# Kernel tuning notes

Measured on AMD Instinct MI355X. Metric: run time of the kernel, lower is better.

The kernel has to match this reference:

```python
import jax, jax.numpy as jnp
import numpy as np

N_NODES = 100000
N_EDGES = 3200000
IN_CH = 256
HID = 256   # 2 * out_channels
OUT = 128


def _gcn_norm(edge_index, n):
    # PyG GCNConv normalization: add self-loops, norm = d^-1/2[src] * d^-1/2[dst]
    src, dst = edge_index[0], edge_index[1]
    loops = jnp.arange(n, dtype=src.dtype)
    src = jnp.concatenate([src, loops])
    dst = jnp.concatenate([dst, loops])
    ones = jnp.ones_like(dst, dtype=jnp.float32)
    deg = jax.ops.segment_sum(ones, dst, num_segments=n)
    dinv = jnp.where(deg > 0, jax.lax.rsqrt(deg), 0.0)
    norm = dinv[src] * dinv[dst]
    return src, dst, norm


def _gcn_conv(x, W, b, src, dst, norm, n):
    h = x @ W                              # [N, F_out] dense transform first (F_out <= F_in)
    msg = h[src] * norm[:, None]           # gather + scale  [E+N, F_out]
    out = jax.ops.segment_sum(msg, dst, num_segments=n)  # scatter-add
    return out + b


def setup_inputs() -> dict:
    key = jax.random.key(0)
    k1, k2, k3, k4 = jax.random.split(key, 4)
    x = jax.random.normal(k1, (N_NODES, IN_CH), dtype=jnp.float32)
    edge_index = jax.random.randint(k2, (2, N_EDGES), 0, N_NODES, dtype=jnp.int64)
    # Glorot-style init for weights, zero bias (PyG GCNConv defaults)
    W1 = jax.random.normal(k3, (IN_CH, HID), dtype=jnp.float32) * (1.0 / np.sqrt(IN_CH))
    b1 = jnp.zeros((HID,), dtype=jnp.float32)
    W2 = jax.random.normal(k4, (HID, OUT), dtype=jnp.float32) * (1.0 / np.sqrt(HID))
    b2 = jnp.zeros((OUT,), dtype=jnp.float32)
    return {"x": x, "edge_index": edge_index, "W1": W1, "b1": b1, "W2": W2, "b2": b2}


def reference(x, edge_index, W1, b1, W2, b2):
    n = x.shape[0]
    src, dst, norm = _gcn_norm(edge_index, n)  # cached=True: shared across both layers
    h = _gcn_conv(x, W1, b1, src, dst, norm, n)
    h = jax.nn.relu(h)
    z = _gcn_conv(h, W2, b2, src, dst, norm, n)
    return z
```

## Files before the change

kernel.cpp:

```cpp
#include <hip/hip_runtime.h>
#include <cstdio>


#define NPB 256
#define PCHUNK 8192

typedef _Float16 half4v __attribute__((ext_vector_type(4)));
typedef _Float16 half8v __attribute__((ext_vector_type(8)));
typedef float    f32x4  __attribute__((ext_vector_type(4)));
typedef float    f32x8  __attribute__((ext_vector_type(8)));

__global__ __launch_bounds__(256) void k_bhist(const int* __restrict__ dst,
                                               int* __restrict__ bcnt,
                                               int e, int nb) {
  __shared__ int h[512];
  for (int i = threadIdx.x; i < nb; i += 256) h[i] = 0;
  __syncthreads();
  int c0 = blockIdx.x * PCHUNK;
  int c1 = min(c0 + PCHUNK, e);
  for (int i = c0 + threadIdx.x; i < c1; i += 256)
    atomicAdd(&h[dst[i] >> 8], 1);
  __syncthreads();
  for (int i = threadIdx.x; i < nb; i += 256)
    if (h[i]) atomicAdd(&bcnt[i], h[i]);
}

__global__ __launch_bounds__(512) void k_bscan(const int* __restrict__ bcnt,
                                               int* __restrict__ bbase,
                                               int* __restrict__ gcur, int nb) {
  __shared__ int sm[512];
  int tid = threadIdx.x;
  sm[tid] = (tid < nb) ? bcnt[tid] : 0;
  __syncthreads();
  for (int d = 1; d < 512; d <<= 1) {
    int t = (tid >= d) ? sm[tid - d] : 0;
    __syncthreads();
    sm[tid] += t;
    __syncthreads();
  }
  int ex = (tid == 0) ? 0 : sm[tid - 1];
  if (tid < nb) {
    bbase[tid] = ex;
    gcur[tid] = ex;
  }
  if (tid == nb) bbase[nb] = sm[nb - 1];
}

__global__ __launch_bounds__(256) void k_partition(const int* __restrict__ src,
                                                   const int* __restrict__ dst,
                                                   int* __restrict__ gcur,
                                                   uint2* __restrict__ tmp,
                                                   int e, int nb) {
  __shared__ int hist[512];
  __shared__ int base[512];
  for (int i = threadIdx.x; i < nb; i += 256) hist[i] = 0;
  __syncthreads();
  int c0 = blockIdx.x * PCHUNK;
  int c1 = min(c0 + PCHUNK, e);
  for (int i = c0 + threadIdx.x; i < c1; i += 256)
    atomicAdd(&hist[dst[i] >> 8], 1);
  __syncthreads();
  for (int i = threadIdx.x; i < nb; i += 256) {
    int c = hist[i];
    base[i] = c ? atomicAdd(&gcur[i], c) : 0;
    hist[i] = 0;
  }
  __syncthreads();
  for (int i = c0 + threadIdx.x; i < c1; i += 256) {
    int d = dst[i];
    int b = d >> 8;
    int pos = base[b] + atomicAdd(&hist[b], 1);
    uint2 v;
    v.x = (unsigned)src[i];
    v.y = (unsigned)d;
    tmp[pos] = v;
  }
}

__global__ __launch_bounds__(256) void k_bucket(const uint2* __restrict__ tmp,
                                                const int* __restrict__ bbase,
                                                int* __restrict__ off,
                                                float* __restrict__ dinv,
                                                int* __restrict__ esrc, int n) {
  __shared__ int lcnt[NPB];
  __shared__ int lsum[NPB];
  __shared__ int lcur[NPB];
  const int b = blockIdx.x;
  const int tid = threadIdx.x;
  const int r0 = b << 8;
  const int nn = min(NPB, n - r0);
  const int lo = bbase[b], hi = bbase[b + 1];

  lcnt[tid] = 0;
  __syncthreads();
  for (int i = lo + tid; i < hi; i += 256)
    atomicAdd(&lcnt[tmp[i].y & (NPB - 1)], 1);
  __syncthreads();
  lsum[tid] = lcnt[tid];
  __syncthreads();
  for (int d = 1; d < NPB; d <<= 1) {
    int t = (tid >= d) ? lsum[tid - d] : 0;
    __syncthreads();
    lsum[tid] += t;
    __syncthreads();
  }
  int ex = (tid == 0) ? 0 : lsum[tid - 1];
  if (tid < nn) {
    off[r0 + tid] = lo + ex;
    dinv[r0 + tid] = rsqrtf((float)(lcnt[tid] + 1));
    lcur[tid] = lo + ex;
  }
  if (r0 + nn == n && tid == 0) off[n] = hi;
  __syncthreads();
  for (int i = lo + tid; i < hi; i += 256) {
    uint2 t2 = tmp[i];
    int pos = atomicAdd(&lcur[t2.y & (NPB - 1)], 1);
    esrc[pos] = (int)t2.x;
  }
}

__global__ __launch_bounds__(256) void k_castWT(const float* __restrict__ W,
                                                _Float16* __restrict__ WhT,
                                                _Float16* __restrict__ WlT,
                                                int K, int N) {
  int i = blockIdx.x * 256 + threadIdx.x;
  if (i >= K * N) return;
  int n = i % N, k = i / N;
  float v = W[i];
  _Float16 h = (_Float16)v;
  WhT[(size_t)n * K + k] = h;
  WlT[(size_t)n * K + k] = (_Float16)(v - (float)h);
}

__global__ __launch_bounds__(256, 2) void k_gemm1(
    const float* __restrict__ A, const _Float16* __restrict__ BhT,
    const _Float16* __restrict__ BlT, _Float16* __restrict__ C,
    int M, int N, int K) {
  __shared__ _Float16 Ah[128][40];
  __shared__ _Float16 Al[128][40];

  const int tid = threadIdx.x;
  const int bm = blockIdx.x * 128;

  const int arow = tid >> 1;
  const int acol = (tid & 1) * 16;
  const bool avalid = (bm + arow) < M;
  const float* aptr = A + (size_t)(bm + arow) * K + acol;

  const int wave = tid >> 6, lane = tid & 63;
  const int wm = (wave & 1) * 64, wn = (wave >> 1) * 128;
  const int lr = lane & 15, quad = lane >> 4;

  const _Float16* bh0 = BhT + (size_t)(wn + lr) * K + quad * 8;
  const _Float16* bl0 = BlT + (size_t)(wn + lr) * K + quad * 8;

  f32x4 acc[4][8] = {};

  for (int k0 = 0; k0 < K; k0 += 32) {
    __syncthreads();
    if (avalid) {
#pragma unroll
      for (int ii = 0; ii < 4; ++ii) {
        f32x4 v = *(const f32x4*)(aptr + k0 + ii * 4);
        half4v hv, lv;
#pragma unroll
        for (int j = 0; j < 4; ++j) {
          hv[j] = (_Float16)v[j];
          lv[j] = (_Float16)(v[j] - (float)hv[j]);
        }
        *(half4v*)&Ah[arow][acol + ii * 4] = hv;
        *(half4v*)&Al[arow][acol + ii * 4] = lv;
      }
    } else {
      half4v z = {};
#pragma unroll
      for (int ii = 0; ii < 4; ++ii) {
        *(half4v*)&Ah[arow][acol + ii * 4] = z;
        *(half4v*)&Al[arow][acol + ii * 4] = z;
      }
    }
    __syncthreads();

    half8v af[4], alf[4];
#pragma unroll
    for (int mi = 0; mi < 4; ++mi) {
      af[mi] = *(const half8v*)&Ah[wm + mi * 16 + lr][quad * 8];
      alf[mi] = *(const half8v*)&Al[wm + mi * 16 + lr][quad * 8];
    }
#pragma unroll
    for (int ni = 0; ni < 8; ++ni) {
      half8v bh = *(const half8v*)(bh0 + (size_t)(ni * 16) * K + k0);
      half8v bl = *(const half8v*)(bl0 + (size_t)(ni * 16) * K + k0);
#pragma unroll
      for (int mi = 0; mi < 4; ++mi) {
        acc[mi][ni] = __builtin_amdgcn_mfma_f32_16x16x32_f16(
            af[mi], bh, acc[mi][ni], 0, 0, 0);
        acc[mi][ni] = __builtin_amdgcn_mfma_f32_16x16x32_f16(
            af[mi], bl, acc[mi][ni], 0, 0, 0);
        acc[mi][ni] = __builtin_amdgcn_mfma_f32_16x16x32_f16(
            alf[mi], bh, acc[mi][ni], 0, 0, 0);
      }
    }
  }

#pragma unroll
  for (int mi = 0; mi < 4; ++mi)
#pragma unroll
    for (int r = 0; r < 4; ++r) {
      int row = bm + wm + mi * 16 + quad * 4 + r;
      if (row < M) {
#pragma unroll
        for (int ni = 0; ni < 8; ++ni)
          C[(size_t)row * N + wn + ni * 16 + lr] = (_Float16)acc[mi][ni][r];
      }
    }
}

template <typename AT, int NTERMS>
__global__ __launch_bounds__(256, 2) void k_gemm_mfma(
    const AT* __restrict__ A, const _Float16* __restrict__ BhT,
    const _Float16* __restrict__ BlT, _Float16* __restrict__ C,
    int M, int N, int K) {
  constexpr bool SPLITA = (NTERMS == 3);
  __shared__ _Float16 Ah[128][40];
  __shared__ _Float16 Al[SPLITA ? 128 : 1][40];

  const int tid = threadIdx.x;
  const int bm = blockIdx.x * 128;
  const int bn = blockIdx.y * 128;

  const int arow = tid >> 1;
  const int acol = (tid & 1) * 16;
  const bool avalid = (bm + arow) < M;
  const AT* aptr = A + (size_t)(bm + arow) * K + acol;

  const int wave = tid >> 6, lane = tid & 63;
  const int wm = (wave & 1) * 64, wn = (wave >> 1) * 64;
  const int lr = lane & 15, quad = lane >> 4;

  const _Float16* bh0 = BhT + (size_t)(bn + wn + lr) * K + quad * 8;
  const _Float16* bl0 = BlT + (size_t)(bn + wn + lr) * K + quad * 8;

  f32x4 acc[4][4] = {};

  for (int k0 = 0; k0 < K; k0 += 32) {
    __syncthreads();
    if (avalid) {
#pragma unroll
      for (int ii = 0; ii < 4; ++ii) {
        if constexpr (SPLITA) {
          f32x4 v = *(const f32x4*)(aptr + k0 + ii * 4);
          half4v hv, lv;
#pragma unroll
          for (int j = 0; j < 4; ++j) {
            hv[j] = (_Float16)v[j];
            lv[j] = (_Float16)(v[j] - (float)hv[j]);
          }
          *(half4v*)&Ah[arow][acol + ii * 4] = hv;
          *(half4v*)&Al[arow][acol + ii * 4] = lv;
        } else {
          half4v v = *(const half4v*)(aptr + k0 + ii * 4);
          *(half4v*)&Ah[arow][acol + ii * 4] = v;
        }
      }
    } else {
      half4v z = {};
#pragma unroll
      for (int ii = 0; ii < 4; ++ii) {
        *(half4v*)&Ah[arow][acol + ii * 4] = z;
        if constexpr (SPLITA) *(half4v*)&Al[arow][acol + ii * 4] = z;
      }
    }
    __syncthreads();

    half8v af[4], alf[4], bhf[4], blf[4];
#pragma unroll
    for (int mi = 0; mi < 4; ++mi) {
      af[mi] = *(const half8v*)&Ah[wm + mi * 16 + lr][quad * 8];
      if constexpr (SPLITA)
        alf[mi] = *(const half8v*)&Al[wm + mi * 16 + lr][quad * 8];
    }
#pragma unroll
    for (int ni = 0; ni < 4; ++ni) {
      bhf[ni] = *(const half8v*)(bh0 + (size_t)(ni * 16) * K + k0);
      blf[ni] = *(const half8v*)(bl0 + (size_t)(ni * 16) * K + k0);
    }
#pragma unroll
    for (int mi = 0; mi < 4; ++mi)
#pragma unroll
      for (int ni = 0; ni < 4; ++ni) {
        acc[mi][ni] = __builtin_amdgcn_mfma_f32_16x16x32_f16(
            af[mi], bhf[ni], acc[mi][ni], 0, 0, 0);
        acc[mi][ni] = __builtin_amdgcn_mfma_f32_16x16x32_f16(
            af[mi], blf[ni], acc[mi][ni], 0, 0, 0);
        if constexpr (SPLITA)
          acc[mi][ni] = __builtin_amdgcn_mfma_f32_16x16x32_f16(
              alf[mi], bhf[ni], acc[mi][ni], 0, 0, 0);
      }
  }

#pragma unroll
  for (int mi = 0; mi < 4; ++mi)
#pragma unroll
    for (int r = 0; r < 4; ++r) {
      int row = bm + wm + mi * 16 + quad * 4 + r;
      if (row < M) {
#pragma unroll
        for (int ni = 0; ni < 4; ++ni)
          C[(size_t)row * N + bn + wn + ni * 16 + lr] =
              (_Float16)acc[mi][ni][r];
      }
    }
}

template <int C, bool RELU, typename OutT>
__global__ __launch_bounds__(256) void k_agg(const _Float16* __restrict__ h,
                                             const int* __restrict__ esrc,
                                             const int* __restrict__ off,
                                             const float* __restrict__ dinv,
                                             const float* __restrict__ bias,
                                             OutT* __restrict__ out, int n) {
  constexpr int LPE = C / 8;
  constexpr int EPL = 64 / LPE;
  constexpr int U = 4;
  int gwave = (blockIdx.x * 256 + threadIdx.x) >> 6;
  int lane = threadIdx.x & 63;
  if (gwave >= n) return;
  const int i = gwave;
  const int eslot = lane / LPE;
  const int sub = lane % LPE;
  const float di = dinv[i];
  const _Float16* hb = h + sub * 8;

  f32x8 acc = {};
  if (eslot == 0)
    acc = di * __builtin_convertvector(*(const half8v*)(hb + (size_t)i * C),
                                       f32x8);

  int e = off[i];
  const int e1 = off[i + 1];
  for (; e + U * EPL <= e1; e += U * EPL) {
    int s[U];
#pragma unroll
    for (int g = 0; g < U; ++g) s[g] = esrc[e + g * EPL + eslot];
    float w[U];
    half8v v[U];
#pragma unroll
    for (int g = 0; g < U; ++g) {
      w[g] = dinv[s[g]];
      v[g] = *(const half8v*)(hb + (size_t)s[g] * C);
    }
#pragma unroll
    for (int g = 0; g < U; ++g)
      acc += w[g] * __builtin_convertvector(v[g], f32x8);
  }
  for (; e < e1; e += EPL) {
    int eg = e + eslot;
    if (eg < e1) {
      int s = esrc[eg];
      acc += dinv[s] * __builtin_convertvector(
                           *(const half8v*)(hb + (size_t)s * C), f32x8);
    }
  }

#pragma unroll
  for (int j = 0; j < 8; ++j) {
    float t = acc[j];
#pragma unroll
    for (int m = LPE; m < 64; m <<= 1) t += __shfl_xor(t, m);
    acc[j] = t;
  }

  if (eslot == 0) {
    f32x8 bv = *(const f32x8*)(bias + sub * 8);
    f32x8 r = acc * di + bv;
    if (RELU) {
#pragma unroll
      for (int j = 0; j < 8; ++j) r[j] = fmaxf(r[j], 0.f);
    }
    if constexpr (sizeof(OutT) == 2) {
      *(half8v*)(out + (size_t)i * C + sub * 8) =
          __builtin_convertvector(r, half8v);
    } else {
      *(f32x8*)(out + (size_t)i * C + sub * 8) = r;
    }
  }
}

extern "C" void kernel_launch(void* const* d_in, const int* in_sizes, int n_in,
                              void* d_out, int out_size, void* d_ws, size_t ws_size,
                              hipStream_t stream) {
  const float* x  = (const float*)d_in[0];
  const int*   ei = (const int*)d_in[1];
  const float* W1 = (const float*)d_in[2];
  const float* b1 = (const float*)d_in[3];
  const float* W2 = (const float*)d_in[4];
  const float* b2 = (const float*)d_in[5];
  float* out = (float*)d_out;

  const int IN_CH = 256, HID = 256, OUT = 128;
  const int N = in_sizes[0] / IN_CH;
  const int E = in_sizes[1] / 2;
  const int* src = ei;
  const int* dst = ei + E;
  const int NB = (N + NPB - 1) / NPB;

  char* p = (char*)d_ws;
  auto alloc = [&](size_t bytes) {
    void* r = (void*)p;
    p += (bytes + 255) & ~(size_t)255;
    return r;
  };
  _Float16* h1   = (_Float16*)alloc((size_t)N * HID * 2);
  _Float16* h1r  = (_Float16*)alloc((size_t)N * HID * 2);
  int*      esrc = (int*)alloc((size_t)E * 4);
  uint2*    tmp  = (uint2*)alloc((size_t)E * 8);
  int*      off  = (int*)alloc((size_t)(N + 1) * 4);
  float*    dinv = (float*)alloc((size_t)N * 4);
  int*      bcnt = (int*)alloc((size_t)(NB + 1) * 4);
  int*      bbase= (int*)alloc((size_t)(NB + 1) * 4);
  int*      gcur = (int*)alloc((size_t)(NB + 1) * 4);
  _Float16* w1h  = (_Float16*)alloc((size_t)IN_CH * HID * 2);
  _Float16* w1l  = (_Float16*)alloc((size_t)IN_CH * HID * 2);
  _Float16* w2h  = (_Float16*)alloc((size_t)HID * OUT * 2);
  _Float16* w2l  = (_Float16*)alloc((size_t)HID * OUT * 2);
  if ((size_t)(p - (char*)d_ws) > ws_size) {
    fprintf(stderr, "kernel_launch: ws too small (need %zu, have %zu)\n",
            (size_t)(p - (char*)d_ws), ws_size);
    return;
  }

  const int nBlkP = (E + PCHUNK - 1) / PCHUNK;

  hipMemsetAsync(bcnt, 0, (size_t)(NB + 1) * 4, stream);
  k_bhist<<<nBlkP, 256, 0, stream>>>(dst, bcnt, E, NB);
  k_bscan<<<1, 512, 0, stream>>>(bcnt, bbase, gcur, NB);
  k_partition<<<nBlkP, 256, 0, stream>>>(src, dst, gcur, tmp, E, NB);
  k_bucket<<<NB, 256, 0, stream>>>(tmp, bbase, off, dinv, esrc, N);
  k_castWT<<<(IN_CH * HID + 255) / 256, 256, 0, stream>>>(W1, w1h, w1l, IN_CH, HID);
  k_castWT<<<(HID * OUT + 255) / 256, 256, 0, stream>>>(W2, w2h, w2l, HID, OUT);
  k_gemm1<<<(N + 127) / 128, 256, 0, stream>>>(x, w1h, w1l, h1, N, HID, IN_CH);
  int aggBlk = (N + 3) / 4;
  k_agg<256, true, _Float16><<<aggBlk, 256, 0, stream>>>(h1, esrc, off, dinv, b1, h1r, N);
  dim3 g2((N + 127) / 128, OUT / 128);
  k_gemm_mfma<_Float16, 2><<<g2, 256, 0, stream>>>(h1r, w2h, w2l, h1, N, OUT, HID);
  k_agg<128, false, float><<<aggBlk, 256, 0, stream>>>(h1, esrc, off, dinv, b2, out, N);
}
```

Baseline: 744.3 us.

## Split GCN aggregation into 64-channel passes and use finer dst buckets

The neighbour aggregation now runs as several launches, each gathering only a 64-channel slice of the features. This shrinks the per-pass gather working set so more of the random row gathers can hit in cache. The price is rereading the edge lists and dinv once per pass and paying extra launch overhead. The CSR build also moves to 64-node buckets with smaller partition chunks, and the bucket scan now handles more buckets than threads.

```diff
diff --git a/kernel.cpp b/kernel.cpp
--- a/kernel.cpp
+++ b/kernel.cpp
@@ -2,8 +2,9 @@
 #include <cstdio>
 
 
-#define NPB 256
-#define PCHUNK 8192
+#define NPB 64
+#define PCHUNK 2048
+#define MAXB 1664
 
 typedef _Float16 half4v __attribute__((ext_vector_type(4)));
 typedef _Float16 half8v __attribute__((ext_vector_type(8)));
@@ -13,13 +14,13 @@
 __global__ __launch_bounds__(256) void k_bhist(const int* __restrict__ dst,
                                                int* __restrict__ bcnt,
                                                int e, int nb) {
-  __shared__ int h[512];
+  __shared__ int h[MAXB];
   for (int i = threadIdx.x; i < nb; i += 256) h[i] = 0;
   __syncthreads();
   int c0 = blockIdx.x * PCHUNK;
   int c1 = min(c0 + PCHUNK, e);
   for (int i = c0 + threadIdx.x; i < c1; i += 256)
-    atomicAdd(&h[dst[i] >> 8], 1);
+    atomicAdd(&h[dst[i] >> 6], 1);
   __syncthreads();
   for (int i = threadIdx.x; i < nb; i += 256)
     if (h[i]) atomicAdd(&bcnt[i], h[i]);
@@ -27,10 +28,16 @@
 
 __global__ __launch_bounds__(512) void k_bscan(const int* __restrict__ bcnt,
                                                int* __restrict__ bbase,
-                                               int* __restrict__ gcur, int nb) {
+                                               int* __restrict__ gcur,
+                                               int nb) {
   __shared__ int sm[512];
-  int tid = threadIdx.x;
-  sm[tid] = (tid < nb) ? bcnt[tid] : 0;
+  const int tid = threadIdx.x;
+  const int chunk = (nb + 511) >> 9;
+  const int c0 = min(tid * chunk, nb);
+  const int c1 = min(c0 + chunk, nb);
+  int sum = 0;
+  for (int j = c0; j < c1; ++j) sum += bcnt[j];
+  sm[tid] = sum;
   __syncthreads();
   for (int d = 1; d < 512; d <<= 1) {
     int t = (tid >= d) ? sm[tid - d] : 0;
@@ -38,12 +45,13 @@
     sm[tid] += t;
     __syncthreads();
   }
-  int ex = (tid == 0) ? 0 : sm[tid - 1];
-  if (tid < nb) {
-    bbase[tid] = ex;
-    gcur[tid] = ex;
-  }
-  if (tid == nb) bbase[nb] = sm[nb - 1];
+  int run = (tid == 0) ? 0 : sm[tid - 1];
+  for (int j = c0; j < c1; ++j) {
+    bbase[j] = run;
+    gcur[j] = run;
+    run += bcnt[j];
+  }
+  if (tid == 511) bbase[nb] = run;
 }
 
 __global__ __launch_bounds__(256) void k_partition(const int* __restrict__ src,
@@ -51,14 +59,14 @@
                                                    int* __restrict__ gcur,
                                                    uint2* __restrict__ tmp,
                                                    int e, int nb) {
-  __shared__ int hist[512];
-  __shared__ int base[512];
+  __shared__ int hist[MAXB];
+  __shared__ int base[MAXB];
   for (int i = threadIdx.x; i < nb; i += 256) hist[i] = 0;
   __syncthreads();
   int c0 = blockIdx.x * PCHUNK;
   int c1 = min(c0 + PCHUNK, e);
   for (int i = c0 + threadIdx.x; i < c1; i += 256)
-    atomicAdd(&hist[dst[i] >> 8], 1);
+    atomicAdd(&hist[dst[i] >> 6], 1);
   __syncthreads();
   for (int i = threadIdx.x; i < nb; i += 256) {
     int c = hist[i];
@@ -68,7 +76,7 @@
   __syncthreads();
   for (int i = c0 + threadIdx.x; i < c1; i += 256) {
     int d = dst[i];
-    int b = d >> 8;
+    int b = d >> 6;
     int pos = base[b] + atomicAdd(&hist[b], 1);
     uint2 v;
     v.x = (unsigned)src[i];
@@ -87,24 +95,24 @@
   __shared__ int lcur[NPB];
   const int b = blockIdx.x;
   const int tid = threadIdx.x;
-  const int r0 = b << 8;
+  const int r0 = b << 6;
   const int nn = min(NPB, n - r0);
   const int lo = bbase[b], hi = bbase[b + 1];
 
-  lcnt[tid] = 0;
+  if (tid < NPB) lcnt[tid] = 0;
   __syncthreads();
   for (int i = lo + tid; i < hi; i += 256)
     atomicAdd(&lcnt[tmp[i].y & (NPB - 1)], 1);
   __syncthreads();
-  lsum[tid] = lcnt[tid];
+  if (tid < NPB) lsum[tid] = lcnt[tid];
   __syncthreads();
   for (int d = 1; d < NPB; d <<= 1) {
-    int t = (tid >= d) ? lsum[tid - d] : 0;
-    __syncthreads();
-    lsum[tid] += t;
-    __syncthreads();
-  }
-  int ex = (tid == 0) ? 0 : lsum[tid - 1];
+    int t = (tid >= d && tid < NPB) ? lsum[tid - d] : 0;
+    __syncthreads();
+    if (tid < NPB) lsum[tid] += t;
+    __syncthreads();
+  }
+  int ex = (tid == 0) ? 0 : ((tid < NPB) ? lsum[tid - 1] : 0);
   if (tid < nn) {
     off[r0 + tid] = lo + ex;
     dinv[r0 + tid] = rsqrtf((float)(lcnt[tid] + 1));
@@ -313,14 +321,15 @@
     }
 }
 
-template <int C, bool RELU, typename OutT>
+template <int C, int CPP, bool RELU, typename OutT>
 __global__ __launch_bounds__(256) void k_agg(const _Float16* __restrict__ h,
                                              const int* __restrict__ esrc,
                                              const int* __restrict__ off,
                                              const float* __restrict__ dinv,
                                              const float* __restrict__ bias,
-                                             OutT* __restrict__ out, int n) {
-  constexpr int LPE = C / 8;
+                                             OutT* __restrict__ out, int n,
+                                             int pass) {
+  constexpr int LPE = CPP / 8;
   constexpr int EPL = 64 / LPE;
   constexpr int U = 4;
   int gwave = (blockIdx.x * 256 + threadIdx.x) >> 6;
@@ -330,7 +339,7 @@
   const int eslot = lane / LPE;
   const int sub = lane % LPE;
   const float di = dinv[i];
-  const _Float16* hb = h + sub * 8;
+  const _Float16* hb = h + (size_t)pass * CPP + sub * 8;
 
   f32x8 acc = {};
   if (eslot == 0)
@@ -372,17 +381,17 @@
   }
 
   if (eslot == 0) {
-    f32x8 bv = *(const f32x8*)(bias + sub * 8);
+    f32x8 bv = *(const f32x8*)(bias + pass * CPP + sub * 8);
     f32x8 r = acc * di + bv;
     if (RELU) {
 #pragma unroll
       for (int j = 0; j < 8; ++j) r[j] = fmaxf(r[j], 0.f);
     }
     if constexpr (sizeof(OutT) == 2) {
-      *(half8v*)(out + (size_t)i * C + sub * 8) =
+      *(half8v*)(out + (size_t)i * C + pass * CPP + sub * 8) =
           __builtin_convertvector(r, half8v);
     } else {
-      *(f32x8*)(out + (size_t)i * C + sub * 8) = r;
+      *(f32x8*)(out + (size_t)i * C + pass * CPP + sub * 8) = r;
     }
   }
 }
@@ -441,8 +450,12 @@
   k_castWT<<<(HID * OUT + 255) / 256, 256, 0, stream>>>(W2, w2h, w2l, HID, OUT);
   k_gemm1<<<(N + 127) / 128, 256, 0, stream>>>(x, w1h, w1l, h1, N, HID, IN_CH);
   int aggBlk = (N + 3) / 4;
-  k_agg<256, true, _Float16><<<aggBlk, 256, 0, stream>>>(h1, esrc, off, dinv, b1, h1r, N);
+  for (int pass = 0; pass < 4; ++pass)
+    k_agg<256, 64, true, _Float16><<<aggBlk, 256, 0, stream>>>(
+        h1, esrc, off, dinv, b1, h1r, N, pass);
   dim3 g2((N + 127) / 128, OUT / 128);
   k_gemm_mfma<_Float16, 2><<<g2, 256, 0, stream>>>(h1r, w2h, w2l, h1, N, OUT, HID);
-  k_agg<128, false, float><<<aggBlk, 256, 0, stream>>>(h1, esrc, off, dinv, b2, out, N);
-}
+  for (int pass = 0; pass < 2; ++pass)
+    k_agg<128, 64, false, float><<<aggBlk, 256, 0, stream>>>(
+        h1, esrc, off, dinv, b2, out, N, pass);
+}
```

After: 846.6 us. +13.8%, slower.
